# Performance work log

Measured on AMD Instinct MI355X. Metric: run time of the kernel, lower is better.

Reference implementation:

```python
import jax, jax.numpy as jnp
import numpy as np

D = 1024
LN_EPS = 1e-5


def setup_inputs() -> dict:
    key = jax.random.key(0)
    k1, k2 = jax.random.split(key)
    L, B = 2048, 8
    x = jax.random.normal(k1, (L, B, D), dtype=jnp.float32)
    c = jnp.zeros((B, D), dtype=jnp.float32)
    W = jax.random.normal(k2, (3 * D, D), dtype=jnp.float32) * (1.0 / np.sqrt(D))
    # bias: forget-gate slice [D:2D] initialized to 1.5, rest zero (matches _init_bias)
    b = jnp.zeros((3 * D,), dtype=jnp.float32).at[D:2 * D].set(1.5)
    ln_g = jnp.ones((D,), dtype=jnp.float32)
    ln_b = jnp.zeros((D,), dtype=jnp.float32)
    return {"x": x, "c": c, "W": W, "b": b, "ln_g": ln_g, "ln_b": ln_b}


def _layernorm(x, g, b):
    mu = jnp.mean(x, axis=-1, keepdims=True)
    var = jnp.mean(jnp.square(x - mu), axis=-1, keepdims=True)
    return (x - mu) * jax.lax.rsqrt(var + LN_EPS) * g + b


def _sru_forward(x, c, W, b, ln_g, ln_b):
    residual = x
    x_norm = _layernorm(x, ln_g, ln_b)          # [L, B, D]
    ufr = jnp.einsum('lbd,ed->lbe', x_norm, W) + b  # [L, B, 3D]
    u, f, r = jnp.split(ufr, 3, axis=-1)
    f_gate = jax.nn.sigmoid(f)
    r_gate = jax.nn.sigmoid(r)
    u_tanh = jnp.tanh(u)

    def step(c_prev, inputs):
        f_t, u_t = inputs
        c_t = f_t * c_prev + (1.0 - f_t) * u_t
        return c_t, c_t

    last_c, c_stack = jax.lax.scan(step, c, (f_gate, u_tanh))  # [L, B, D]
    hs = r_gate * jnp.tanh(c_stack) + (1.0 - r_gate) * x_norm
    return residual + hs, last_c


def reference(x, c, W, b, ln_g, ln_b):
    return _sru_forward(x, c, W, b, ln_g, ln_b)
```

## Files before the change

kernel.cpp:

```cpp
#include <hip/hip_runtime.h>

#define L_DIM 2048
#define B_DIM 8
#define DD    1024
#define M_DIM 16384
#define N_DIM 3072
#define K_DIM 1024
#define CH    8192
#define CH8   1024
#define NSEG  128
#define LSEG  16
#define LN_EPS 1e-5f

typedef __attribute__((ext_vector_type(8))) short bf16x8;
typedef __attribute__((ext_vector_type(8))) unsigned short u16x8;
typedef __attribute__((ext_vector_type(4))) float f32x4;

__device__ __forceinline__ unsigned short f2bf(float f){
  unsigned u = __float_as_uint(f);
  u += 0x7fffu + ((u >> 16) & 1u);
  return (unsigned short)(u >> 16);
}
__device__ __forceinline__ float bf2f(unsigned short h){
  return __uint_as_float(((unsigned)h) << 16);
}
__device__ __forceinline__ float fsigmoid(float z){ return 1.0f/(1.0f + __expf(-z)); }
__device__ __forceinline__ float ftanh(float z){ return 1.0f - 2.0f/(1.0f + __expf(2.0f*z)); }

__global__ __launch_bounds__(256) void ln_kernel(const float* __restrict__ x,
                                                 const float* __restrict__ g,
                                                 const float* __restrict__ bta,
                                                 unsigned short* __restrict__ xn)
{
  int tid  = threadIdx.x;
  int wave = tid >> 6, lane = tid & 63;
  int row  = blockIdx.x * 4 + wave;
  const float4* xr = (const float4*)(x + (size_t)row * DD);
  float4 v[4];
  #pragma unroll
  for (int k = 0; k < 4; k++) v[k] = xr[lane + k * 64];
  float s = 0.f, sq = 0.f;
  #pragma unroll
  for (int k = 0; k < 4; k++) {
    s  += v[k].x + v[k].y + v[k].z + v[k].w;
    sq += v[k].x*v[k].x + v[k].y*v[k].y + v[k].z*v[k].z + v[k].w*v[k].w;
  }
  #pragma unroll
  for (int off = 32; off > 0; off >>= 1) {
    s  += __shfl_down(s,  off, 64);
    sq += __shfl_down(sq, off, 64);
  }
  s  = __shfl(s,  0, 64);
  sq = __shfl(sq, 0, 64);
  float mean = s * (1.0f / DD);
  float var  = sq * (1.0f / DD) - mean * mean;
  float rstd = rsqrtf(var + LN_EPS);
  ushort4* xo = (ushort4*)(xn + (size_t)row * DD);
  #pragma unroll
  for (int k = 0; k < 4; k++) {
    float4 gg = ((const float4*)g)[lane + k * 64];
    float4 bb = ((const float4*)bta)[lane + k * 64];
    ushort4 o;
    o.x = f2bf((v[k].x - mean) * rstd * gg.x + bb.x);
    o.y = f2bf((v[k].y - mean) * rstd * gg.y + bb.y);
    o.z = f2bf((v[k].z - mean) * rstd * gg.z + bb.z);
    o.w = f2bf((v[k].w - mean) * rstd * gg.w + bb.w);
    xo[lane + k * 64] = o;
  }
}

__global__ __launch_bounds__(256) void wconv_kernel(const float* __restrict__ W,
                                                    unsigned short* __restrict__ wb)
{
  int gid = blockIdx.x * 256 + threadIdx.x;
  float4 v = ((const float4*)W)[gid];
  ushort4 o;
  o.x = f2bf(v.x); o.y = f2bf(v.y); o.z = f2bf(v.z); o.w = f2bf(v.w);
  ((ushort4*)wb)[gid] = o;
}

#define BM 256
#define BN 256
#define BK 64
#define NT 16
#define LDPE 264

#define GLDS16(gp, lp) __builtin_amdgcn_global_load_lds( \
    (const __attribute__((address_space(1))) void*)(gp), \
    (__attribute__((address_space(3))) void*)(lp), 16, 0, 0)

#define SBAR()   __builtin_amdgcn_s_barrier()
#define SCHED0() __builtin_amdgcn_sched_barrier(0)
#define WAIT_LGKM0() do { asm volatile("s_waitcnt lgkmcnt(0)" ::: "memory"); SCHED0(); } while(0)
#define WAIT_VM(N)   do { asm volatile("s_waitcnt vmcnt(" #N ")" ::: "memory"); SCHED0(); } while(0)

#define DSR(dst, addr, IMM) \
  asm volatile("ds_read_b128 %0, %1 offset:" #IMM : "=v"(dst) : "v"(addr))

__global__ __launch_bounds__(512, 2) void gemm_gates(const unsigned short* __restrict__ Ag,
                                                     const unsigned short* __restrict__ Bg,
                                                     const float* __restrict__ bias,
                                                     unsigned short* __restrict__ u_t,
                                                     unsigned short* __restrict__ f_g,
                                                     unsigned short* __restrict__ r_g)
{
  __shared__ unsigned short smem[65536];
  const int tid  = threadIdx.x;
  const int wave = tid >> 6, lane = tid & 63;
  const int wm = wave >> 2, wn = wave & 3;
  const int r8 = lane >> 3;
  const int sch = (lane & 7) ^ r8;
  const int fm = lane & 15, quad = lane >> 4, f7 = fm & 7;
  const int bm0 = blockIdx.x * BM, bn0 = blockIdx.y * BN;

  f32x4 zero = {0.f, 0.f, 0.f, 0.f};
  f32x4 acc[8][4];
  #pragma unroll
  for (int i = 0; i < 8; i++)
    #pragma unroll
    for (int j = 0; j < 4; j++) acc[i][j] = zero;

#define STAGE_A(BUF, T, HALF) do { \
  GLDS16(Ag + (size_t)(bm0 + (HALF)*128 + wave*16 + 0 + r8) * K_DIM + ((T)*BK + sch*8), \
         &smem[(BUF)*16384 + ((HALF)*128 + wave*16 + 0) * 64]); \
  GLDS16(Ag + (size_t)(bm0 + (HALF)*128 + wave*16 + 8 + r8) * K_DIM + ((T)*BK + sch*8), \
         &smem[(BUF)*16384 + ((HALF)*128 + wave*16 + 8) * 64]); \
} while(0)

#define STAGE_B(BUF, T, HALF) do { \
  GLDS16(Bg + (size_t)(bn0 + (HALF)*128 + wave*16 + 0 + r8) * K_DIM + ((T)*BK + sch*8), \
         &smem[32768 + (BUF)*16384 + ((HALF)*128 + wave*16 + 0) * 64]); \
  GLDS16(Bg + (size_t)(bn0 + (HALF)*128 + wave*16 + 8 + r8) * K_DIM + ((T)*BK + sch*8), \
         &smem[32768 + (BUF)*16384 + ((HALF)*128 + wave*16 + 8) * 64]); \
} while(0)

#define RD_A(CBB, MH) do { \
  unsigned a0 = (CBB) + aBase + (MH)*8192; unsigned a1 = a0 ^ 64u; \
  DSR(a_[0][0], a0, 0);    DSR(a_[0][1], a1, 0); \
  DSR(a_[1][0], a0, 2048); DSR(a_[1][1], a1, 2048); \
  DSR(a_[2][0], a0, 4096); DSR(a_[2][1], a1, 4096); \
  DSR(a_[3][0], a0, 6144); DSR(a_[3][1], a1, 6144); \
} while(0)

#define RD_B(CBB, NH, D) do { \
  unsigned b0a = (CBB) + bBase + (NH)*4096; unsigned b1a = b0a ^ 64u; \
  DSR(D[0][0], b0a, 0);    DSR(D[0][1], b1a, 0); \
  DSR(D[1][0], b0a, 2048); DSR(D[1][1], b1a, 2048); \
} while(0)

#define QMFMA(MH, NH, BREG) do { \
  _Pragma("unroll") for (int i_ = 0; i_ < 4; ++i_) \
  _Pragma("unroll") for (int j_ = 0; j_ < 2; ++j_) \
  _Pragma("unroll") for (int kk_ = 0; kk_ < 2; ++kk_) \
    acc[(MH)*4 + i_][(NH)*2 + j_] = __builtin_amdgcn_mfma_f32_16x16x32_bf16( \
        a_[i_][kk_], BREG[j_][kk_], acc[(MH)*4 + i_][(NH)*2 + j_], 0, 0, 0); \
} while(0)

  bf16x8 a_[4][2], b0_[2][2], b1_[2][2];
  const unsigned slot0 = (unsigned)((quad ^ f7) << 4);
  const unsigned aBase = (unsigned)((wm * 128 + fm) * 128) + slot0;
  const unsigned bBase = 65536u + (unsigned)((wn * 64 + fm) * 128) + slot0;

  STAGE_A(0, 0, 0); STAGE_A(0, 0, 1);
  STAGE_B(0, 0, 0); STAGE_B(0, 0, 1);
  STAGE_B(1, 1, 0); STAGE_B(1, 1, 1);
  STAGE_A(1, 1, 0);
  WAIT_VM(6);
  SBAR();

  #pragma unroll
  for (int t = 0; t < NT; ++t) {
    const int cb = t & 1, nb = cb ^ 1;
    const unsigned cbB = (unsigned)(cb * 32768);
    RD_A(cbB, 0);
    RD_B(cbB, 0, b0_);
    if (t + 1 < NT) STAGE_A(nb, t + 1, 1);
    SCHED0(); SBAR();
    WAIT_LGKM0();
    __builtin_amdgcn_s_setprio(1);
    QMFMA(0, 0, b0_);
    __builtin_amdgcn_s_setprio(0);
    SBAR();
    RD_B(cbB, 1, b1_);
    SCHED0(); SBAR();
    WAIT_LGKM0();
    __builtin_amdgcn_s_setprio(1);
    QMFMA(0, 1, b1_);
    __builtin_amdgcn_s_setprio(0);
    SBAR();
    RD_A(cbB, 1);
    if (t + 2 < NT) STAGE_B(cb, t + 2, 0);
    SCHED0(); SBAR();
    WAIT_LGKM0();
    __builtin_amdgcn_s_setprio(1);
    QMFMA(1, 1, b1_);
    __builtin_amdgcn_s_setprio(0);
    SBAR();
    if (t + 2 < NT) { STAGE_B(cb, t + 2, 1); STAGE_A(cb, t + 2, 0); }
    SCHED0();
    __builtin_amdgcn_s_setprio(1);
    QMFMA(1, 0, b0_);
    __builtin_amdgcn_s_setprio(0);
    if (t < NT - 2)       WAIT_VM(6);
    else if (t == NT - 2) WAIT_VM(0);
    SBAR();
  }
  __syncthreads();

  const int slice = bn0 >> 10;
  const int nd0   = bn0 & 1023;
  unsigned short* dst = (slice == 0) ? u_t : ((slice == 1) ? f_g : r_g);

  #pragma unroll
  for (int h = 0; h < 2; ++h) {
    if (wm == h) {
      #pragma unroll
      for (int ni = 0; ni < 4; ++ni) {
        int lcol = wn * 64 + ni * 16 + fm;
        float bia = bias[bn0 + lcol];
        #pragma unroll
        for (int mi = 0; mi < 8; ++mi) {
          #pragma unroll
          for (int reg = 0; reg < 4; ++reg) {
            int lrow = mi * 16 + quad * 4 + reg;
            float v = acc[mi][ni][reg] + bia;
            float act = (slice == 0) ? ftanh(v) : fsigmoid(v);
            smem[lrow * LDPE + lcol] = f2bf(act);
          }
        }
      }
    }
    __syncthreads();
    #pragma unroll
    for (int it = 0; it < 8; ++it) {
      int row = it * 16 + (tid >> 5);
      int cc  = (tid & 31) * 8;
      u16x8 v = *(const u16x8*)&smem[row * LDPE + cc];
      *(u16x8*)(dst + (size_t)(bm0 + h * 128 + row) * DD + nd0 + cc) = v;
    }
    __syncthreads();
  }
}

__global__ __launch_bounds__(256) void scan_pass1(const unsigned short* __restrict__ f_g,
                                                  const unsigned short* __restrict__ u_t,
                                                  unsigned short* __restrict__ P,
                                                  unsigned short* __restrict__ E)
{
  int vc8 = blockIdx.x * 256 + threadIdx.x;
  int seg = blockIdx.y;
  const u16x8* f8 = (const u16x8*)f_g;
  const u16x8* u8 = (const u16x8*)u_t;
  size_t g = (size_t)(seg * LSEG) * CH8 + vc8;
  float p[8], e[8];
  #pragma unroll
  for (int k = 0; k < 8; k++) { p[k] = 1.f; e[k] = 0.f; }
  #pragma unroll 4
  for (int i = 0; i < LSEG; i++) {
    u16x8 ff = f8[g];
    u16x8 uu = u8[g];
    #pragma unroll
    for (int k = 0; k < 8; k++) {
      float fv = bf2f(ff[k]);
      e[k] = fv * e[k] + (1.f - fv) * bf2f(uu[k]);
      p[k] *= fv;
    }
    g += CH8;
  }
  u16x8 pv, ev;
  #pragma unroll
  for (int k = 0; k < 8; k++) { pv[k] = f2bf(p[k]); ev[k] = f2bf(e[k]); }
  ((u16x8*)P)[(size_t)seg * CH8 + vc8] = pv;
  ((u16x8*)E)[(size_t)seg * CH8 + vc8] = ev;
}

__global__ __launch_bounds__(128) void scan_pass2(const unsigned short* __restrict__ P,
                                                  const unsigned short* __restrict__ E,
                                                  const float* __restrict__ c0,
                                                  float* __restrict__ Cini,
                                                  float* __restrict__ lastc)
{
  int ch = blockIdx.x * 128 + threadIdx.x;
  float c = c0[ch];
  #pragma unroll 8
  for (int s = 0; s < NSEG; s++) {
    Cini[(size_t)s * CH + ch] = c;
    c = bf2f(P[(size_t)s * CH + ch]) * c + bf2f(E[(size_t)s * CH + ch]);
  }
  lastc[ch] = c;
}

__global__ __launch_bounds__(256) void scan_pass3(const unsigned short* __restrict__ f_g,
                                                  const unsigned short* __restrict__ u_t,
                                                  const unsigned short* __restrict__ r_g,
                                                  const float* __restrict__ x,
                                                  const unsigned short* __restrict__ xn,
                                                  const float* __restrict__ Cini,
                                                  float* __restrict__ out)
{
  int vc8 = blockIdx.x * 256 + threadIdx.x;
  int seg = blockIdx.y;
  const u16x8* f8 = (const u16x8*)f_g;
  const u16x8* u8 = (const u16x8*)u_t;
  const u16x8* r8 = (const u16x8*)r_g;
  const u16x8* n8 = (const u16x8*)xn;
  const float4* x4 = (const float4*)x;
  float4* o4 = (float4*)out;
  float c[8];
  {
    const float4* C4 = (const float4*)Cini;
    size_t ci = (size_t)seg * (CH / 4) + (size_t)vc8 * 2;
    float4 ca = C4[ci], cb = C4[ci + 1];
    c[0]=ca.x; c[1]=ca.y; c[2]=ca.z; c[3]=ca.w;
    c[4]=cb.x; c[5]=cb.y; c[6]=cb.z; c[7]=cb.w;
  }
  size_t g = (size_t)(seg * LSEG) * CH8 + vc8;
  #pragma unroll 2
  for (int i = 0; i < LSEG; i++) {
    u16x8 ff = f8[g];
    u16x8 uu = u8[g];
    u16x8 rr = r8[g];
    u16x8 nn = n8[g];
    size_t xi = g * 2;
    float4 xa = x4[xi], xb = x4[xi + 1];
    float ov[8];
    #pragma unroll
    for (int k = 0; k < 8; k++) {
      float fv = bf2f(ff[k]);
      c[k] = fv * c[k] + (1.f - fv) * bf2f(uu[k]);
      float rv = bf2f(rr[k]);
      ov[k] = rv * ftanh(c[k]) + (1.f - rv) * bf2f(nn[k]);
    }
    o4[xi]     = (float4){xa.x + ov[0], xa.y + ov[1], xa.z + ov[2], xa.w + ov[3]};
    o4[xi + 1] = (float4){xb.x + ov[4], xb.y + ov[5], xb.z + ov[6], xb.w + ov[7]};
    g += CH8;
  }
}

extern "C" void kernel_launch(void* const* d_in, const int* in_sizes, int n_in,
                              void* d_out, int out_size, void* d_ws, size_t ws_size,
                              hipStream_t stream) {
  const float* x    = (const float*)d_in[0];
  const float* c0   = (const float*)d_in[1];
  const float* W    = (const float*)d_in[2];
  const float* bias = (const float*)d_in[3];
  const float* ln_g = (const float*)d_in[4];
  const float* ln_b = (const float*)d_in[5];
  float* out = (float*)d_out;

  char* ws = (char*)d_ws;
  unsigned short* xn  = (unsigned short*)(ws);
  unsigned short* wb  = (unsigned short*)(ws + 33554432ULL);
  unsigned short* u_t = (unsigned short*)(ws + 39845888ULL);
  unsigned short* f_g = (unsigned short*)(ws + 73400320ULL);
  unsigned short* r_g = (unsigned short*)(ws + 106954752ULL);
  unsigned short* Pseg = (unsigned short*)(ws + 33554432ULL);
  unsigned short* Eseg = (unsigned short*)(ws + 35651584ULL);
  float* Cini = (float*)(ws + 140509184ULL);

  ln_kernel   <<<M_DIM / 4, 256, 0, stream>>>(x, ln_g, ln_b, xn);
  wconv_kernel<<<N_DIM, 256, 0, stream>>>(W, wb);
  gemm_gates  <<<dim3(M_DIM / BM, N_DIM / BN), 512, 0, stream>>>(xn, wb, bias, u_t, f_g, r_g);
  scan_pass1  <<<dim3(CH8 / 256, NSEG), 256, 0, stream>>>(f_g, u_t, Pseg, Eseg);
  scan_pass2  <<<CH / 128, 128, 0, stream>>>(Pseg, Eseg, c0, Cini, out + (size_t)M_DIM * DD);
  scan_pass3  <<<dim3(CH8 / 256, NSEG), 256, 0, stream>>>(f_g, u_t, r_g, x, xn, Cini, out);
}
```

Measured before the change: 237.8 us.

## Interleave LDS fragment reads with MFMA quadrants in GEMM main loop

Restructures the GEMM inner loop so LDS reads for the next quadrant's A/B fragments are issued between groups of MFMAs of the current quadrant. The next tile's first A and B fragments are prefetched during the last quadrant, and fewer barriers sit between loads and compute. This aims to hide LDS latency behind matrix-core work, at the cost of tighter register-reuse ordering and more reliance on the explicit scheduling barriers.

```diff
diff --git a/kernel.cpp b/kernel.cpp
--- a/kernel.cpp
+++ b/kernel.cpp
@@ -134,26 +134,11 @@
          &smem[32768 + (BUF)*16384 + ((HALF)*128 + wave*16 + 8) * 64]); \
 } while(0)
 
-#define RD_A(CBB, MH) do { \
-  unsigned a0 = (CBB) + aBase + (MH)*8192; unsigned a1 = a0 ^ 64u; \
-  DSR(a_[0][0], a0, 0);    DSR(a_[0][1], a1, 0); \
-  DSR(a_[1][0], a0, 2048); DSR(a_[1][1], a1, 2048); \
-  DSR(a_[2][0], a0, 4096); DSR(a_[2][1], a1, 4096); \
-  DSR(a_[3][0], a0, 6144); DSR(a_[3][1], a1, 6144); \
-} while(0)
-
-#define RD_B(CBB, NH, D) do { \
-  unsigned b0a = (CBB) + bBase + (NH)*4096; unsigned b1a = b0a ^ 64u; \
-  DSR(D[0][0], b0a, 0);    DSR(D[0][1], b1a, 0); \
-  DSR(D[1][0], b0a, 2048); DSR(D[1][1], b1a, 2048); \
-} while(0)
-
-#define QMFMA(MH, NH, BREG) do { \
-  _Pragma("unroll") for (int i_ = 0; i_ < 4; ++i_) \
-  _Pragma("unroll") for (int j_ = 0; j_ < 2; ++j_) \
-  _Pragma("unroll") for (int kk_ = 0; kk_ < 2; ++kk_) \
-    acc[(MH)*4 + i_][(NH)*2 + j_] = __builtin_amdgcn_mfma_f32_16x16x32_bf16( \
-        a_[i_][kk_], BREG[j_][kk_], acc[(MH)*4 + i_][(NH)*2 + j_], 0, 0, 0); \
+#define MFMA4_Q(MH, NH, BREG, I) do { \
+  acc[(MH)*4+(I)][(NH)*2+0] = __builtin_amdgcn_mfma_f32_16x16x32_bf16(a_[I][0], BREG[0][0], acc[(MH)*4+(I)][(NH)*2+0], 0,0,0); \
+  acc[(MH)*4+(I)][(NH)*2+0] = __builtin_amdgcn_mfma_f32_16x16x32_bf16(a_[I][1], BREG[0][1], acc[(MH)*4+(I)][(NH)*2+0], 0,0,0); \
+  acc[(MH)*4+(I)][(NH)*2+1] = __builtin_amdgcn_mfma_f32_16x16x32_bf16(a_[I][0], BREG[1][0], acc[(MH)*4+(I)][(NH)*2+1], 0,0,0); \
+  acc[(MH)*4+(I)][(NH)*2+1] = __builtin_amdgcn_mfma_f32_16x16x32_bf16(a_[I][1], BREG[1][1], acc[(MH)*4+(I)][(NH)*2+1], 0,0,0); \
 } while(0)
 
   bf16x8 a_[4][2], b0_[2][2], b1_[2][2];
@@ -167,42 +152,80 @@
   STAGE_A(1, 1, 0);
   WAIT_VM(6);
   SBAR();
+  {
+    unsigned qa0 = aBase, qa1 = aBase ^ 64u;
+    DSR(a_[0][0], qa0, 0);    DSR(a_[0][1], qa1, 0);
+    DSR(a_[1][0], qa0, 2048); DSR(a_[1][1], qa1, 2048);
+    DSR(a_[2][0], qa0, 4096); DSR(a_[2][1], qa1, 4096);
+    DSR(a_[3][0], qa0, 6144); DSR(a_[3][1], qa1, 6144);
+    unsigned qb0 = bBase, qb1 = bBase ^ 64u;
+    DSR(b0_[0][0], qb0, 0);    DSR(b0_[0][1], qb1, 0);
+    DSR(b0_[1][0], qb0, 2048); DSR(b0_[1][1], qb1, 2048);
+  }
+  SCHED0();
 
   #pragma unroll
   for (int t = 0; t < NT; ++t) {
     const int cb = t & 1, nb = cb ^ 1;
     const unsigned cbB = (unsigned)(cb * 32768);
-    RD_A(cbB, 0);
-    RD_B(cbB, 0, b0_);
+    const unsigned nbB = (unsigned)(nb * 32768);
+
+    WAIT_LGKM0();
     if (t + 1 < NT) STAGE_A(nb, t + 1, 1);
-    SCHED0(); SBAR();
+    SCHED0();
+    __builtin_amdgcn_s_setprio(1);
+    {
+      unsigned q0 = cbB + bBase + 4096u, q1 = q0 ^ 64u;
+      MFMA4_Q(0,0,b0_,0); SCHED0(); DSR(b1_[0][0], q0, 0);    DSR(b1_[0][1], q1, 0);    SCHED0();
+      MFMA4_Q(0,0,b0_,1); SCHED0(); DSR(b1_[1][0], q0, 2048); DSR(b1_[1][1], q1, 2048); SCHED0();
+      MFMA4_Q(0,0,b0_,2); SCHED0();
+      MFMA4_Q(0,0,b0_,3);
+    }
+    __builtin_amdgcn_s_setprio(0);
+    SCHED0();
+    SBAR();
+
     WAIT_LGKM0();
     __builtin_amdgcn_s_setprio(1);
-    QMFMA(0, 0, b0_);
+    {
+      unsigned q0 = cbB + aBase + 8192u, q1 = q0 ^ 64u;
+      MFMA4_Q(0,1,b1_,0); SCHED0(); DSR(a_[0][0], q0, 0);    DSR(a_[0][1], q1, 0);    SCHED0();
+      MFMA4_Q(0,1,b1_,1); SCHED0(); DSR(a_[1][0], q0, 2048); DSR(a_[1][1], q1, 2048); SCHED0();
+      MFMA4_Q(0,1,b1_,2); SCHED0(); DSR(a_[2][0], q0, 4096); DSR(a_[2][1], q1, 4096); SCHED0();
+      MFMA4_Q(0,1,b1_,3); SCHED0(); DSR(a_[3][0], q0, 6144); DSR(a_[3][1], q1, 6144); SCHED0();
+    }
     __builtin_amdgcn_s_setprio(0);
+    SCHED0();
     SBAR();
-    RD_B(cbB, 1, b1_);
-    SCHED0(); SBAR();
+
     WAIT_LGKM0();
+    if (t + 2 < NT) STAGE_B(cb, t + 2, 0);
+    SCHED0();
     __builtin_amdgcn_s_setprio(1);
-    QMFMA(0, 1, b1_);
+    MFMA4_Q(1,1,b1_,0); MFMA4_Q(1,1,b1_,1); MFMA4_Q(1,1,b1_,2); MFMA4_Q(1,1,b1_,3);
     __builtin_amdgcn_s_setprio(0);
+    SCHED0();
     SBAR();
-    RD_A(cbB, 1);
-    if (t + 2 < NT) STAGE_B(cb, t + 2, 0);
-    SCHED0(); SBAR();
-    WAIT_LGKM0();
-    __builtin_amdgcn_s_setprio(1);
-    QMFMA(1, 1, b1_);
-    __builtin_amdgcn_s_setprio(0);
-    SBAR();
+
     if (t + 2 < NT) { STAGE_B(cb, t + 2, 1); STAGE_A(cb, t + 2, 0); }
     SCHED0();
-    __builtin_amdgcn_s_setprio(1);
-    QMFMA(1, 0, b0_);
-    __builtin_amdgcn_s_setprio(0);
     if (t < NT - 2)       WAIT_VM(6);
     else if (t == NT - 2) WAIT_VM(0);
+    __builtin_amdgcn_s_setprio(1);
+    {
+      unsigned q0 = nbB + aBase, q1 = q0 ^ 64u;
+      MFMA4_Q(1,0,b0_,0); SCHED0(); if (t+1 < NT) { DSR(a_[0][0], q0, 0);    DSR(a_[0][1], q1, 0);    } SCHED0();
+      MFMA4_Q(1,0,b0_,1); SCHED0(); if (t+1 < NT) { DSR(a_[1][0], q0, 2048); DSR(a_[1][1], q1, 2048); } SCHED0();
+      MFMA4_Q(1,0,b0_,2); SCHED0(); if (t+1 < NT) { DSR(a_[2][0], q0, 4096); DSR(a_[2][1], q1, 4096); } SCHED0();
+      MFMA4_Q(1,0,b0_,3); SCHED0(); if (t+1 < NT) { DSR(a_[3][0], q0, 6144); DSR(a_[3][1], q1, 6144); } SCHED0();
+    }
+    __builtin_amdgcn_s_setprio(0);
+    if (t + 1 < NT) {
+      unsigned q0 = nbB + bBase, q1 = q0 ^ 64u;
+      DSR(b0_[0][0], q0, 0);    DSR(b0_[0][1], q1, 0);
+      DSR(b0_[1][0], q0, 2048); DSR(b0_[1][1], q1, 2048);
+    }
+    SCHED0();
     SBAR();
   }
   __syncthreads();
```

Result: faster. 232.5 us (-2.2%).
